# Kernel optimization log

Measured on AMD Instinct MI355X. Metric: run time of the kernel, lower is better.

## Reference

```python
import jax, jax.numpy as jnp
import numpy as np

B, NUM, LENTH, AUX = 32, 64, 64, 64
SIZE, OUT = 256, 256
IN_G = (LENTH + 1) * 2 + AUX  # 194


def _linear_params(k, fan_in, fan_out):
    # torch nn.Linear default init: U(-1/sqrt(fan_in), 1/sqrt(fan_in))
    s = 1.0 / np.sqrt(fan_in)
    kw, kb = jax.random.split(k)
    W = jax.random.uniform(kw, (fan_in, fan_out), minval=-s, maxval=s, dtype=jnp.float32)
    b = jax.random.uniform(kb, (fan_out,), minval=-s, maxval=s, dtype=jnp.float32)
    return W, b


def setup_inputs() -> dict:
    key = jax.random.key(0)
    ks = jax.random.split(key, 8)
    inp = {"x_aux": jax.random.normal(ks[0], (B, NUM, LENTH + AUX), dtype=jnp.float32)}
    dims = [("g1", IN_G, SIZE), ("g2", SIZE, SIZE), ("g3", SIZE, SIZE), ("g4", SIZE, OUT),
            ("f1", OUT, SIZE), ("f2", SIZE, SIZE), ("f3", SIZE, OUT)]
    for k, (name, fi, fo) in zip(ks[1:], dims):
        W, b = _linear_params(k, fi, fo)
        inp[name + "_w"] = W
        inp[name + "_b"] = b
    return inp


def reference(x_aux, g1_w, g1_b, g2_w, g2_b, g3_w, g3_b, g4_w, g4_b,
              f1_w, f1_b, f2_w, f2_b, f3_w, f3_b):
    bsz = x_aux.shape[0]
    # coord feature = object index i
    coord = jnp.broadcast_to(
        jnp.arange(NUM, dtype=x_aux.dtype)[None, :, None], (bsz, NUM, 1))
    x = jnp.concatenate([x_aux[:, :, :LENTH], coord], axis=-1)      # [B, N, LENTH+1]
    xa = jnp.concatenate([x_aux, coord], axis=-1)                   # [B, N, LENTH+AUX+1]
    # all-pairs broadcast+concat -> [B, N, N, IN_G]
    x_i = jnp.broadcast_to(x[:, None, :, :], (bsz, NUM, NUM, LENTH + 1))
    x_j = jnp.broadcast_to(xa[:, :, None, :], (bsz, NUM, NUM, LENTH + AUX + 1))
    pairs = jnp.concatenate([x_i, x_j], axis=-1)
    # shared g-MLP over every pair
    h = jax.nn.relu(pairs @ g1_w + g1_b)
    h = jax.nn.relu(h @ g2_w + g2_b)
    h = jax.nn.relu(h @ g3_w + g3_b)
    h = jax.nn.relu(h @ g4_w + g4_b)
    # sum-pool over all N*N pairs -> [B, OUT]
    x_g = h.sum(axis=(1, 2))
    # f-MLP (dropout treated as identity / eval mode)
    x_f = jax.nn.relu(x_g @ f1_w + f1_b)
    x_f = jax.nn.relu(x_f @ f2_w + f2_b)
    return x_f @ f3_w + f3_b
```

## Files before the change

### kernel.cpp

```cpp
#include <hip/hip_runtime.h>

#define BATCH 32
#define NOBJ  64
#define PADK  264

typedef _Float16 f16x4 __attribute__((ext_vector_type(4)));
typedef _Float16 f16x8 __attribute__((ext_vector_type(8)));
typedef float    f32x4 __attribute__((ext_vector_type(4)));
typedef float    f32x16 __attribute__((ext_vector_type(16)));

#define MFMA32(a, b, c) __builtin_amdgcn_mfma_f32_32x32x16_f16((a), (b), (c), 0, 0, 0)

__global__ __launch_bounds__(256) void prep_weights(
    const float* __restrict__ g1w, const float* __restrict__ g2w,
    const float* __restrict__ g3w, const float* __restrict__ g4w,
    _Float16* __restrict__ wtf, float* __restrict__ xg) {
  __shared__ _Float16 tile[256][33];
  const int blk = blockIdx.x;
  const int t = threadIdx.x;
  xg[blk * 256 + t] = 0.0f;

  const int l  = blk >> 3;
  const int nt = blk & 7;
  const float* src = (l == 0) ? g1w : (l == 1) ? g2w : (l == 2) ? g3w : g4w;

  const int nn = t & 31, kb = t >> 5;
#pragma unroll 4
  for (int pass = 0; pass < 32; ++pass) {
    int kn = pass * 8 + kb;
    int ok;
    if (l == 0) {
      if (kn < 64)        ok = kn;
      else if (kn < 192)  ok = kn + 1;
      else if (kn == 192) ok = 64;
      else if (kn == 193) ok = 193;
      else                ok = -1;
    } else {
      ok = kn;
    }
    float v = (ok >= 0) ? src[(size_t)ok * 256 + nt * 32 + nn] : 0.0f;
    tile[kn][nn] = (_Float16)v;
  }
  __syncthreads();

  const int lane = t & 63;
  const int nfrag = lane & 31;
  const int kbase = (lane >> 5) * 8;
  _Float16* dst = wtf + ((size_t)(l * 8 + nt) * 16) * 512;
#pragma unroll
  for (int q = 0; q < 4; ++q) {
    int kk = (t >> 6) + 4 * q;
    f16x8 fr;
#pragma unroll
    for (int j = 0; j < 8; ++j)
      fr[j] = tile[kk * 16 + kbase + j][nfrag];
    *(f16x8*)(dst + (size_t)kk * 512 + lane * 8) = fr;
  }
}

template <int STEPS>
__device__ __forceinline__ void gemm_2x2(
    const _Float16* bp0, const _Float16* bp1,
    const _Float16* ar0, const _Float16* ar1,
    f32x16& acc00, f32x16& acc10, f32x16& acc01, f32x16& acc11) {
  f16x8 b0 = *(const f16x8*)bp0;
  f16x8 b1 = *(const f16x8*)bp1;
#pragma unroll
  for (int kk = 0; kk < STEPS; ++kk) {
    f16x8 a0 = *(const f16x8*)(ar0 + kk * 16);
    f16x8 a1 = *(const f16x8*)(ar1 + kk * 16);
    f16x8 nb0 = b0, nb1 = b1;
    if (kk < STEPS - 1) {
      nb0 = *(const f16x8*)(bp0 + (kk + 1) * 512);
      nb1 = *(const f16x8*)(bp1 + (kk + 1) * 512);
    }
    acc00 = MFMA32(a0, b0, acc00);
    acc10 = MFMA32(a1, b0, acc10);
    acc01 = MFMA32(a0, b1, acc01);
    acc11 = MFMA32(a1, b1, acc11);
    b0 = nb0; b1 = nb1;
  }
}

__global__ __launch_bounds__(512, 4) void g_mlp_pool(
    const float* __restrict__ x_aux,
    const _Float16* __restrict__ wtf,
    const float* __restrict__ g1b, const float* __restrict__ g2b,
    const float* __restrict__ g3b, const float* __restrict__ g4b,
    float* __restrict__ xg) {
  __shared__ _Float16 As[128][PADK];

  const int b  = blockIdx.x >> 5;
  const int i0 = (blockIdx.x & 31) * 2;
  const int t  = threadIdx.x;

  {
    const float* xb = x_aux + (size_t)b * NOBJ * 128;
    {
      const int c4 = t & 15, r0 = t >> 4;
#pragma unroll
      for (int it = 0; it < 4; ++it) {
        int r = it * 32 + r0;
        f32x4 v = *(const f32x4*)(xb + (size_t)(r & 63) * 128 + c4 * 4);
        f16x4 hh = {(_Float16)v[0], (_Float16)v[1], (_Float16)v[2], (_Float16)v[3]};
        *(f16x4*)&As[r][c4 * 4] = hh;
      }
    }
    {
      const int row = t >> 2, seg = t & 3;
      const int ir = i0 + (row >> 6);
      const float* xi = xb + (size_t)ir * 128;
#pragma unroll
      for (int u = 0; u < 4; ++u) {
        int c = seg * 32 + u * 8;
        f32x4 v0 = *(const f32x4*)(xi + c);
        f32x4 v1 = *(const f32x4*)(xi + c + 4);
        f16x8 hh = {(_Float16)v0[0], (_Float16)v0[1], (_Float16)v0[2], (_Float16)v0[3],
                    (_Float16)v1[0], (_Float16)v1[1], (_Float16)v1[2], (_Float16)v1[3]};
        *(f16x8*)&As[row][64 + c] = hh;
      }
      f16x8 z = {};
      *(f16x8*)&As[row][192 + seg * 16]     = z;
      *(f16x8*)&As[row][192 + seg * 16 + 8] = z;
      if (seg == 0) {
        As[row][192] = (_Float16)(row & 63);
        As[row][193] = (_Float16)ir;
      }
    }
  }
  __syncthreads();

  const int lane = t & 63;
  const int wave = t >> 6;
  const int mh   = wave & 1;
  const int nq   = wave >> 1;
  const int c31  = lane & 31;
  const int h    = lane >> 5;
  const int n0   = nq * 64;
  const int R    = mh * 64;
  const float* gb[4] = {g1b, g2b, g3b, g4b};

  for (int layer = 0; layer < 4; ++layer) {
    const float bv0 = gb[layer][n0 + c31];
    const float bv1 = gb[layer][n0 + 32 + c31];

    f32x16 acc00 = {}, acc10 = {}, acc01 = {}, acc11 = {};

    const _Float16* bp0 =
        wtf + ((size_t)(layer * 8 + nq * 2) * 16) * 512 + lane * 8;
    const _Float16* bp1 = bp0 + 16 * 512;
    const _Float16* ar0 = &As[R + c31][h * 8];
    const _Float16* ar1 = &As[R + 32 + c31][h * 8];

    if (layer == 0)
      gemm_2x2<13>(bp0, bp1, ar0, ar1, acc00, acc10, acc01, acc11);
    else
      gemm_2x2<16>(bp0, bp1, ar0, ar1, acc00, acc10, acc01, acc11);

    if (layer < 3) {
      __syncthreads();
#pragma unroll
      for (int g = 0; g < 4; ++g)
#pragma unroll
        for (int r = 0; r < 4; ++r) {
          const int row = g * 8 + h * 4 + r;
          const int reg = g * 4 + r;
          As[R + row][n0 + c31]           = (_Float16)fmaxf(acc00[reg] + bv0, 0.f);
          As[R + 32 + row][n0 + c31]      = (_Float16)fmaxf(acc10[reg] + bv0, 0.f);
          As[R + row][n0 + 32 + c31]      = (_Float16)fmaxf(acc01[reg] + bv1, 0.f);
          As[R + 32 + row][n0 + 32 + c31] = (_Float16)fmaxf(acc11[reg] + bv1, 0.f);
        }
      __syncthreads();
    } else {
      float s0 = 0.f, s1 = 0.f;
#pragma unroll
      for (int reg = 0; reg < 16; ++reg) {
        s0 += fmaxf(acc00[reg] + bv0, 0.f) + fmaxf(acc10[reg] + bv0, 0.f);
        s1 += fmaxf(acc01[reg] + bv1, 0.f) + fmaxf(acc11[reg] + bv1, 0.f);
      }
      s0 += __shfl_xor(s0, 32, 64);
      s1 += __shfl_xor(s1, 32, 64);
      if (h == 0) {
        atomicAdd(&xg[b * 256 + n0 + c31], s0);
        atomicAdd(&xg[b * 256 + n0 + 32 + c31], s1);
      }
    }
  }
}

__global__ __launch_bounds__(1024) void f_mlp(
    const float* __restrict__ xg,
    const float* __restrict__ f1w, const float* __restrict__ f1b,
    const float* __restrict__ f2w, const float* __restrict__ f2b,
    const float* __restrict__ f3w, const float* __restrict__ f3b,
    float* __restrict__ out) {
  __shared__ float xs[256], ys[256], ps[4][256];
  const int b = blockIdx.x;
  const int t = threadIdx.x;
  const int n = t & 255;
  const int kc = t >> 8;

  if (t < 256) xs[t] = xg[b * 256 + t];
  __syncthreads();

  float p = 0.f;
#pragma unroll 8
  for (int k0 = 0; k0 < 64; ++k0) {
    int k = kc * 64 + k0;
    p += xs[k] * f1w[k * 256 + n];
  }
  ps[kc][n] = p;
  __syncthreads();
  if (t < 256)
    ys[t] = fmaxf(f1b[t] + ps[0][t] + ps[1][t] + ps[2][t] + ps[3][t], 0.f);
  __syncthreads();

  p = 0.f;
#pragma unroll 8
  for (int k0 = 0; k0 < 64; ++k0) {
    int k = kc * 64 + k0;
    p += ys[k] * f2w[k * 256 + n];
  }
  ps[kc][n] = p;
  __syncthreads();
  if (t < 256)
    xs[t] = fmaxf(f2b[t] + ps[0][t] + ps[1][t] + ps[2][t] + ps[3][t], 0.f);
  __syncthreads();

  p = 0.f;
#pragma unroll 8
  for (int k0 = 0; k0 < 64; ++k0) {
    int k = kc * 64 + k0;
    p += xs[k] * f3w[k * 256 + n];
  }
  ps[kc][n] = p;
  __syncthreads();
  if (t < 256)
    out[b * 256 + t] = f3b[t] + ps[0][t] + ps[1][t] + ps[2][t] + ps[3][t];
}

extern "C" void kernel_launch(void* const* d_in, const int* in_sizes, int n_in,
                              void* d_out, int out_size, void* d_ws, size_t ws_size,
                              hipStream_t stream) {
  const float* x_aux = (const float*)d_in[0];
  const float* g1w = (const float*)d_in[1];
  const float* g1b = (const float*)d_in[2];
  const float* g2w = (const float*)d_in[3];
  const float* g2b = (const float*)d_in[4];
  const float* g3w = (const float*)d_in[5];
  const float* g3b = (const float*)d_in[6];
  const float* g4w = (const float*)d_in[7];
  const float* g4b = (const float*)d_in[8];
  const float* f1w = (const float*)d_in[9];
  const float* f1b = (const float*)d_in[10];
  const float* f2w = (const float*)d_in[11];
  const float* f2b = (const float*)d_in[12];
  const float* f3w = (const float*)d_in[13];
  const float* f3b = (const float*)d_in[14];
  float* out = (float*)d_out;

  _Float16* wtf = (_Float16*)d_ws;
  float* xg = (float*)((char*)d_ws + 4u * 256u * 256u * 2u);

  hipLaunchKernelGGL(prep_weights, dim3(32), dim3(256), 0, stream,
                     g1w, g2w, g3w, g4w, wtf, xg);
  hipLaunchKernelGGL(g_mlp_pool, dim3(BATCH * 32), dim3(512), 0, stream,
                     x_aux, wtf, g1b, g2b, g3b, g4b, xg);
  hipLaunchKernelGGL(f_mlp, dim3(BATCH), dim3(1024), 0, stream,
                     xg, f1w, f1b, f2w, f2b, f3w, f3b, out);
}
```

Measured before the change: 170.3 us.

## Use 4 waves per block, each computing all 128 rows for 64 columns

Blocks go from 8 waves to 4. Each wave now owns a full 128x64 output tile (8 accumulators) instead of 64x64, so each B weight fragment loaded from global feeds 4 MFMAs instead of 2, halving weight traffic per block. All B fragments for a layer are preloaded into registers before the MFMA loop. This raises register pressure sharply (128 accumulator floats plus up to 32 f16x8 B registers per lane) and reduces waves per block. Launch bounds change to (256,2), which may lower occupancy or cause spills.

```diff
diff --git a/kernel.cpp b/kernel.cpp
--- a/kernel.cpp
+++ b/kernel.cpp
@@ -59,30 +59,27 @@
 }
 
 template <int STEPS>
-__device__ __forceinline__ void gemm_2x2(
-    const _Float16* bp0, const _Float16* bp1,
-    const _Float16* ar0, const _Float16* ar1,
-    f32x16& acc00, f32x16& acc10, f32x16& acc01, f32x16& acc11) {
-  f16x8 b0 = *(const f16x8*)bp0;
-  f16x8 b1 = *(const f16x8*)bp1;
+__device__ __forceinline__ void do_layer(
+    const _Float16* __restrict__ bp0, const _Float16* __restrict__ bp1,
+    const _Float16* __restrict__ arow, f32x16 acc[8]) {
+  f16x8 b0[STEPS], b1[STEPS];
 #pragma unroll
   for (int kk = 0; kk < STEPS; ++kk) {
-    f16x8 a0 = *(const f16x8*)(ar0 + kk * 16);
-    f16x8 a1 = *(const f16x8*)(ar1 + kk * 16);
-    f16x8 nb0 = b0, nb1 = b1;
-    if (kk < STEPS - 1) {
-      nb0 = *(const f16x8*)(bp0 + (kk + 1) * 512);
-      nb1 = *(const f16x8*)(bp1 + (kk + 1) * 512);
-    }
-    acc00 = MFMA32(a0, b0, acc00);
-    acc10 = MFMA32(a1, b0, acc10);
-    acc01 = MFMA32(a0, b1, acc01);
-    acc11 = MFMA32(a1, b1, acc11);
-    b0 = nb0; b1 = nb1;
-  }
-}
-
-__global__ __launch_bounds__(512, 4) void g_mlp_pool(
+    b0[kk] = *(const f16x8*)(bp0 + kk * 512);
+    b1[kk] = *(const f16x8*)(bp1 + kk * 512);
+  }
+#pragma unroll
+  for (int kk = 0; kk < STEPS; ++kk) {
+#pragma unroll
+    for (int m = 0; m < 4; ++m) {
+      f16x8 a = *(const f16x8*)(arow + (size_t)m * 32 * PADK + kk * 16);
+      acc[m * 2]     = MFMA32(a, b0[kk], acc[m * 2]);
+      acc[m * 2 + 1] = MFMA32(a, b1[kk], acc[m * 2 + 1]);
+    }
+  }
+}
+
+__global__ __launch_bounds__(256, 2) void g_mlp_pool(
     const float* __restrict__ x_aux,
     const _Float16* __restrict__ wtf,
     const float* __restrict__ g1b, const float* __restrict__ g2b,
@@ -99,20 +96,20 @@
     {
       const int c4 = t & 15, r0 = t >> 4;
 #pragma unroll
-      for (int it = 0; it < 4; ++it) {
-        int r = it * 32 + r0;
+      for (int it = 0; it < 8; ++it) {
+        int r = it * 16 + r0;
         f32x4 v = *(const f32x4*)(xb + (size_t)(r & 63) * 128 + c4 * 4);
         f16x4 hh = {(_Float16)v[0], (_Float16)v[1], (_Float16)v[2], (_Float16)v[3]};
         *(f16x4*)&As[r][c4 * 4] = hh;
       }
     }
     {
-      const int row = t >> 2, seg = t & 3;
+      const int row = t >> 1, seg = t & 1;
       const int ir = i0 + (row >> 6);
       const float* xi = xb + (size_t)ir * 128;
 #pragma unroll
-      for (int u = 0; u < 4; ++u) {
-        int c = seg * 32 + u * 8;
+      for (int u = 0; u < 8; ++u) {
+        int c = seg * 64 + u * 8;
         f32x4 v0 = *(const f32x4*)(xi + c);
         f32x4 v1 = *(const f32x4*)(xi + c + 4);
         f16x8 hh = {(_Float16)v0[0], (_Float16)v0[1], (_Float16)v0[2], (_Float16)v0[3],
@@ -120,8 +117,8 @@
         *(f16x8*)&As[row][64 + c] = hh;
       }
       f16x8 z = {};
-      *(f16x8*)&As[row][192 + seg * 16]     = z;
-      *(f16x8*)&As[row][192 + seg * 16 + 8] = z;
+      *(f16x8*)&As[row][192 + seg * 32]     = z;
+      *(f16x8*)&As[row][192 + seg * 32 + 8] = z;
       if (seg == 0) {
         As[row][192] = (_Float16)(row & 63);
         As[row][193] = (_Float16)ir;
@@ -132,52 +129,50 @@
 
   const int lane = t & 63;
   const int wave = t >> 6;
-  const int mh   = wave & 1;
-  const int nq   = wave >> 1;
   const int c31  = lane & 31;
   const int h    = lane >> 5;
-  const int n0   = nq * 64;
-  const int R    = mh * 64;
+  const int n0   = wave * 64;
   const float* gb[4] = {g1b, g2b, g3b, g4b};
 
   for (int layer = 0; layer < 4; ++layer) {
     const float bv0 = gb[layer][n0 + c31];
     const float bv1 = gb[layer][n0 + 32 + c31];
 
-    f32x16 acc00 = {}, acc10 = {}, acc01 = {}, acc11 = {};
+    f32x16 acc[8] = {};
 
     const _Float16* bp0 =
-        wtf + ((size_t)(layer * 8 + nq * 2) * 16) * 512 + lane * 8;
+        wtf + ((size_t)(layer * 8 + wave * 2) * 16) * 512 + lane * 8;
     const _Float16* bp1 = bp0 + 16 * 512;
-    const _Float16* ar0 = &As[R + c31][h * 8];
-    const _Float16* ar1 = &As[R + 32 + c31][h * 8];
+    const _Float16* arow = &As[c31][h * 8];
 
     if (layer == 0)
-      gemm_2x2<13>(bp0, bp1, ar0, ar1, acc00, acc10, acc01, acc11);
+      do_layer<13>(bp0, bp1, arow, acc);
     else
-      gemm_2x2<16>(bp0, bp1, ar0, ar1, acc00, acc10, acc01, acc11);
+      do_layer<16>(bp0, bp1, arow, acc);
 
     if (layer < 3) {
       __syncthreads();
 #pragma unroll
-      for (int g = 0; g < 4; ++g)
-#pragma unroll
-        for (int r = 0; r < 4; ++r) {
-          const int row = g * 8 + h * 4 + r;
-          const int reg = g * 4 + r;
-          As[R + row][n0 + c31]           = (_Float16)fmaxf(acc00[reg] + bv0, 0.f);
-          As[R + 32 + row][n0 + c31]      = (_Float16)fmaxf(acc10[reg] + bv0, 0.f);
-          As[R + row][n0 + 32 + c31]      = (_Float16)fmaxf(acc01[reg] + bv1, 0.f);
-          As[R + 32 + row][n0 + 32 + c31] = (_Float16)fmaxf(acc11[reg] + bv1, 0.f);
-        }
+      for (int m = 0; m < 4; ++m)
+#pragma unroll
+        for (int g = 0; g < 4; ++g)
+#pragma unroll
+          for (int r = 0; r < 4; ++r) {
+            const int row = m * 32 + g * 8 + h * 4 + r;
+            const int reg = g * 4 + r;
+            As[row][n0 + c31]      = (_Float16)fmaxf(acc[m * 2][reg] + bv0, 0.f);
+            As[row][n0 + 32 + c31] = (_Float16)fmaxf(acc[m * 2 + 1][reg] + bv1, 0.f);
+          }
       __syncthreads();
     } else {
       float s0 = 0.f, s1 = 0.f;
 #pragma unroll
-      for (int reg = 0; reg < 16; ++reg) {
-        s0 += fmaxf(acc00[reg] + bv0, 0.f) + fmaxf(acc10[reg] + bv0, 0.f);
-        s1 += fmaxf(acc01[reg] + bv1, 0.f) + fmaxf(acc11[reg] + bv1, 0.f);
-      }
+      for (int m = 0; m < 4; ++m)
+#pragma unroll
+        for (int reg = 0; reg < 16; ++reg) {
+          s0 += fmaxf(acc[m * 2][reg] + bv0, 0.f);
+          s1 += fmaxf(acc[m * 2 + 1][reg] + bv1, 0.f);
+        }
       s0 += __shfl_xor(s0, 32, 64);
       s1 += __shfl_xor(s1, 32, 64);
       if (h == 0) {
@@ -264,7 +259,7 @@
 
   hipLaunchKernelGGL(prep_weights, dim3(32), dim3(256), 0, stream,
                      g1w, g2w, g3w, g4w, wtf, xg);
-  hipLaunchKernelGGL(g_mlp_pool, dim3(BATCH * 32), dim3(512), 0, stream,
+  hipLaunchKernelGGL(g_mlp_pool, dim3(BATCH * 32), dim3(256), 0, stream,
                      x_aux, wtf, g1b, g2b, g3b, g4b, xg);
   hipLaunchKernelGGL(f_mlp, dim3(BATCH), dim3(1024), 0, stream,
                      xg, f1w, f1b, f2w, f2b, f3w, f3b, out);
```

After: 164.1 us. 3.6% less time.
